# Kernel tuning notes

Measured on AMD Instinct MI355X. Metric: run time of the kernel, lower is better.

Reference implementation:

```python
import jax, jax.numpy as jnp
import numpy as np

N = 300000
MAX_TORSION = 7
MAX_RIGID = 8
MAX_SS = 3
MAX_ATOM = 24
NRES = 22
EPS = 1e-6


def v_norm_safe(v):
    # normalize last dim with epsilon clamp (torch v_norm_safe analogue)
    return v / jnp.clip(jnp.linalg.norm(v, axis=-1, keepdims=True), EPS)


def combine_operations(X, Y):
    # X, Y: [..., 4, 3] rigid ops (3x3 rotation rows + 1 translation row)
    rot = X[..., :3, :] @ Y[..., :3, :]
    t = jnp.einsum('...ij,...j->...i', X[..., :3, :], Y[..., 3, :]) + X[..., 3, :]
    return jnp.concatenate([rot, t[..., None, :]], axis=-2)


def setup_inputs() -> dict:
    key = jax.random.key(0)
    ks = jax.random.split(key, 9)
    return {
        'output_0': jax.random.normal(ks[0], (N, 2 * MAX_TORSION + MAX_SS, 1), jnp.float32),
        'output_1': jax.random.normal(ks[1], (N, 3, 3), jnp.float32),
        'pos': jax.random.normal(ks[2], (N, 3), jnp.float32),
        'ss': jax.random.randint(ks[3], (N,), 0, MAX_SS),
        'residue_type': jax.random.randint(ks[4], (N,), 0, NRES),
        'rigid_transforms': jax.random.normal(ks[5], (MAX_SS, NRES, MAX_RIGID, 4, 3), jnp.float32),
        'rigid_groups': jax.random.normal(ks[6], (MAX_SS, NRES, MAX_ATOM, 3), jnp.float32),
        'transforms_dep': jax.random.randint(ks[7], (NRES, MAX_RIGID), 0, MAX_RIGID),
        'rigids_dep': jax.random.randint(ks[8], (NRES, MAX_ATOM), 0, MAX_RIGID),
    }


def reference(output_0, output_1, pos, ss, residue_type,
              rigid_transforms, rigid_groups, transforms_dep, rigids_dep):
    # ---- StructureModule.output_to_opr_6D ----
    bb0 = output_1[:, :2]                                   # [N,2,3]
    e0 = v_norm_safe(bb0[:, 0])
    v1 = bb0[:, 1]
    u1 = v1 - e0 * jnp.sum(e0 * v1, axis=-1, keepdims=True)
    e1 = v_norm_safe(u1)
    e2 = jnp.cross(e0, e1)
    rot = jnp.stack([e0, e1, e2], axis=1).swapaxes(-1, -2)  # [N,3,3]
    t = 0.1 * output_1[:, 2][:, None, :]                    # [N,1,3]
    bb = jnp.concatenate([rot, t], axis=1)                  # [N,4,3]
    sc = v_norm_safe(output_0[:, :2 * MAX_TORSION].reshape(-1, MAX_TORSION, 2))

    # ---- build_structure ----
    transforms = rigid_transforms[ss, residue_type]         # [N,8,4,3]
    rigids = rigid_groups[ss, residue_type]                 # [N,24,3]
    tdep = transforms_dep[residue_type]                     # [N,8]
    rdep = rigids_dep[residue_type]                         # [N,24]

    n = output_0.shape[0]
    c, s = sc[..., 0], sc[..., 1]                           # [N,7]
    zr = jnp.zeros_like(c)
    on = jnp.ones_like(c)
    tor_rot = jnp.stack([
        jnp.stack([on, zr, zr], axis=-1),
        jnp.stack([zr, c, -s], axis=-1),
        jnp.stack([zr, s, c], axis=-1),
    ], axis=-2)                                             # [N,7,3,3]
    tor = jnp.concatenate(
        [tor_rot, jnp.zeros((n, MAX_TORSION, 1, 3), output_0.dtype)], axis=2)
    opr0 = jnp.concatenate([bb[:, :3], (bb[:, 3] + pos)[:, None]], axis=1)  # [N,4,3]
    opr = jnp.concatenate([opr0[:, None], tor], axis=1)     # [N,8,4,3]

    opr = combine_operations(transforms, opr)
    for i_tor in range(1, MAX_RIGID):                       # fixed 7-step dependency chain
        prev = jnp.take_along_axis(opr, tdep[:, i_tor][:, None, None, None], axis=1)[:, 0]
        opr = opr.at[:, i_tor].set(combine_operations(prev, opr[:, i_tor]))

    opr_g = jnp.take_along_axis(opr, rdep[:, :, None, None], axis=1)  # [N,24,4,3]
    R = jnp.einsum('naij,naj->nai', opr_g[:, :, :3], rigids) + opr_g[:, :, 3]
    return (R, opr[:, 0])
```

## Files before the change

### kernel.cpp

```cpp
#include <hip/hip_runtime.h>
#include <math.h>

#define NRES 22

__device__ __forceinline__ void sel8(const float (&fr)[8][12], int d, float (&P)[12]) {
    const bool b0 = (d & 1) != 0;
    const bool b1 = (d & 2) != 0;
    const bool b2 = (d & 4) != 0;
#pragma unroll
    for (int k = 0; k < 12; ++k) {
        float a01 = b0 ? fr[1][k] : fr[0][k];
        float a23 = b0 ? fr[3][k] : fr[2][k];
        float a45 = b0 ? fr[5][k] : fr[4][k];
        float a67 = b0 ? fr[7][k] : fr[6][k];
        float b03 = b1 ? a23 : a01;
        float b47 = b1 ? a67 : a45;
        P[k] = b2 ? b47 : b03;
    }
}

__device__ __forceinline__ void apply_point(const float (&F)[12], float x, float y, float z,
                                            float &px, float &py, float &pz) {
    px = fmaf(F[0], x, fmaf(F[1], y, fmaf(F[2], z, F[9])));
    py = fmaf(F[3], x, fmaf(F[4], y, fmaf(F[5], z, F[10])));
    pz = fmaf(F[6], x, fmaf(F[7], y, fmaf(F[8], z, F[11])));
}

extern "C" __global__ __launch_bounds__(256)
void model_kernel(const float* __restrict__ o0,
                  const float* __restrict__ o1,
                  const float* __restrict__ pos,
                  const int*   __restrict__ ssArr,
                  const int*   __restrict__ rtArr,
                  const float* __restrict__ rigT,
                  const float* __restrict__ rigG,
                  const int*   __restrict__ tdepArr,
                  const int*   __restrict__ rdepArr,
                  float* __restrict__ outR,
                  float* __restrict__ outF,
                  int N)
{
    const int res = blockIdx.x * 256 + threadIdx.x;
    if (res >= N) return;

    const int s  = ssArr[res];
    const int rt = rtArr[res];

    float c[7], sn[7];
    const float* o0p = o0 + (size_t)res * 17;
#pragma unroll
    for (int t = 0; t < 7; ++t) {
        float cr = o0p[2 * t], sr = o0p[2 * t + 1];
        float n2 = cr * cr + sr * sr;
        float inv = rsqrtf(fmaxf(n2, 1e-12f));
        c[t]  = cr * inv;
        sn[t] = sr * inv;
    }

    const float* o1p = o1 + (size_t)res * 9;
    float r0x = o1p[0], r0y = o1p[1], r0z = o1p[2];
    float v1x = o1p[3], v1y = o1p[4], v1z = o1p[5];
    float t2x = o1p[6], t2y = o1p[7], t2z = o1p[8];
    float inv0 = rsqrtf(fmaxf(r0x * r0x + r0y * r0y + r0z * r0z, 1e-12f));
    float e0x = r0x * inv0, e0y = r0y * inv0, e0z = r0z * inv0;
    float d01 = e0x * v1x + e0y * v1y + e0z * v1z;
    float u1x = v1x - e0x * d01, u1y = v1y - e0y * d01, u1z = v1z - e0z * d01;
    float inv1 = rsqrtf(fmaxf(u1x * u1x + u1y * u1y + u1z * u1z, 1e-12f));
    float e1x = u1x * inv1, e1y = u1y * inv1, e1z = u1z * inv1;
    float e2x = e0y * e1z - e0z * e1y;
    float e2y = e0z * e1x - e0x * e1z;
    float e2z = e0x * e1y - e0y * e1x;
    const float* pp = pos + (size_t)res * 3;
    float btx = 0.1f * t2x + pp[0];
    float bty = 0.1f * t2y + pp[1];
    float btz = 0.1f * t2z + pp[2];

    const int sr22 = s * NRES + rt;
    const float4* T4 = (const float4*)rigT + (size_t)sr22 * 24;

    float fr[8][12];

    {
        float4 q0 = T4[0], q1 = T4[1], q2 = T4[2];
        float T0[12] = {q0.x, q0.y, q0.z, q0.w, q1.x, q1.y, q1.z, q1.w,
                        q2.x, q2.y, q2.z, q2.w};
#pragma unroll
        for (int i = 0; i < 3; ++i) {
            float a = T0[i * 3 + 0], b = T0[i * 3 + 1], d = T0[i * 3 + 2];
            fr[0][i * 3 + 0] = a * e0x + b * e0y + d * e0z;
            fr[0][i * 3 + 1] = a * e1x + b * e1y + d * e1z;
            fr[0][i * 3 + 2] = a * e2x + b * e2y + d * e2z;
            fr[0][9 + i]     = a * btx + b * bty + d * btz + T0[9 + i];
        }
    }

#pragma unroll
    for (int f = 1; f < 8; ++f) {
        float4 q0 = T4[f * 3 + 0], q1 = T4[f * 3 + 1], q2 = T4[f * 3 + 2];
        float Tf[12] = {q0.x, q0.y, q0.z, q0.w, q1.x, q1.y, q1.z, q1.w,
                        q2.x, q2.y, q2.z, q2.w};
        float cc = c[f - 1], ssn = sn[f - 1];
#pragma unroll
        for (int i = 0; i < 3; ++i) {
            fr[f][i * 3 + 0] = Tf[i * 3 + 0];
            fr[f][i * 3 + 1] = Tf[i * 3 + 1] * cc + Tf[i * 3 + 2] * ssn;
            fr[f][i * 3 + 2] = Tf[i * 3 + 2] * cc - Tf[i * 3 + 1] * ssn;
            fr[f][9 + i]     = Tf[9 + i];
        }
    }

    int tdv[8];
    {
        const int4* tdq = (const int4*)(tdepArr + rt * 8);
        int4 a = tdq[0], b = tdq[1];
        tdv[0] = a.x; tdv[1] = a.y; tdv[2] = a.z; tdv[3] = a.w;
        tdv[4] = b.x; tdv[5] = b.y; tdv[6] = b.z; tdv[7] = b.w;
    }
#pragma unroll
    for (int i = 1; i < 8; ++i) {
        float P[12];
        sel8(fr, tdv[i] & 7, P);
        float Y[12];
#pragma unroll
        for (int k = 0; k < 12; ++k) Y[k] = fr[i][k];
#pragma unroll
        for (int r = 0; r < 3; ++r) {
            float a = P[r * 3 + 0], b = P[r * 3 + 1], d = P[r * 3 + 2];
#pragma unroll
            for (int j = 0; j < 3; ++j)
                fr[i][r * 3 + j] = a * Y[j] + b * Y[3 + j] + d * Y[6 + j];
            fr[i][9 + r] = a * Y[9] + b * Y[10] + d * Y[11] + P[9 + r];
        }
    }

    const float4* G4  = (const float4*)rigG + (size_t)sr22 * 18;
    const int4*   RD4 = (const int4*)(rdepArr + rt * 24);
    float4* OR4 = (float4*)(outR + (size_t)res * 72);
#pragma unroll
    for (int ck = 0; ck < 6; ++ck) {
        int4 rd = RD4[ck];
        float4 g0 = G4[ck * 3 + 0], g1 = G4[ck * 3 + 1], g2 = G4[ck * 3 + 2];
        float P[12];
        float p0x, p0y, p0z, p1x, p1y, p1z, p2x, p2y, p2z, p3x, p3y, p3z;
        sel8(fr, rd.x & 7, P); apply_point(P, g0.x, g0.y, g0.z, p0x, p0y, p0z);
        sel8(fr, rd.y & 7, P); apply_point(P, g0.w, g1.x, g1.y, p1x, p1y, p1z);
        sel8(fr, rd.z & 7, P); apply_point(P, g1.z, g1.w, g2.x, p2x, p2y, p2z);
        sel8(fr, rd.w & 7, P); apply_point(P, g2.y, g2.z, g2.w, p3x, p3y, p3z);
        OR4[ck * 3 + 0] = make_float4(p0x, p0y, p0z, p1x);
        OR4[ck * 3 + 1] = make_float4(p1y, p1z, p2x, p2y);
        OR4[ck * 3 + 2] = make_float4(p2z, p3x, p3y, p3z);
    }

    float4* OF4 = (float4*)(outF + (size_t)res * 12);
    OF4[0] = make_float4(fr[0][0], fr[0][1], fr[0][2], fr[0][3]);
    OF4[1] = make_float4(fr[0][4], fr[0][5], fr[0][6], fr[0][7]);
    OF4[2] = make_float4(fr[0][8], fr[0][9], fr[0][10], fr[0][11]);
}

extern "C" void kernel_launch(void* const* d_in, const int* in_sizes, int n_in,
                              void* d_out, int out_size, void* d_ws, size_t ws_size,
                              hipStream_t stream) {
    const float* o0   = (const float*)d_in[0];
    const float* o1   = (const float*)d_in[1];
    const float* pos  = (const float*)d_in[2];
    const int*   ssA  = (const int*)d_in[3];
    const int*   rtA  = (const int*)d_in[4];
    const float* rigT = (const float*)d_in[5];
    const float* rigG = (const float*)d_in[6];
    const int*   tdep = (const int*)d_in[7];
    const int*   rdep = (const int*)d_in[8];

    const int N = in_sizes[3];
    float* outR = (float*)d_out;
    float* outF = (float*)d_out + (size_t)N * 72;

    const int block = 256;
    const int grid  = (N + block - 1) / block;
    model_kernel<<<grid, block, 0, stream>>>(o0, o1, pos, ssA, rtA, rigT, rigG,
                                             tdep, rdep, outR, outF, N);
}
```

Measured before the change: 187.0 us.

## Stage lookup tables and per-wave I/O through LDS with persistent grid

Copies the rigid transform, rigid group and dependency tables into padded shared memory once per block, and runs a persistent grid-stride loop capped at 512 blocks. Each wave stages its residues' input rows into LDS with coalesced float4 loads, and transposes its output rows through LDS so global stores are coalesced instead of strided per thread. This targets uncoalesced per-thread global access, at the cost of about 80KB of LDS per block, extra LDS traffic and reduced occupancy.

```diff
diff --git a/kernel.cpp b/kernel.cpp
--- a/kernel.cpp
+++ b/kernel.cpp
@@ -2,6 +2,14 @@
 #include <math.h>
 
 #define NRES 22
+
+#define ST_F    0
+#define SG_F    6600
+#define STD_I   11616
+#define SRD_I   11814
+#define TBL_F   12364
+#define CHUNK_F 1856
+#define SMEM_BYTES ((TBL_F + 4 * CHUNK_F) * 4)
 
 __device__ __forceinline__ void sel8(const float (&fr)[8][12], int d, float (&P)[12]) {
     const bool b0 = (d & 1) != 0;
@@ -26,7 +34,20 @@
     pz = fmaf(F[6], x, fmaf(F[7], y, fmaf(F[8], z, F[11])));
 }
 
-extern "C" __global__ __launch_bounds__(256)
+__device__ __forceinline__ void wave_stage(const float* __restrict__ src, float* dst,
+                                           int nF, int lane) {
+    const int n4 = nF >> 2;
+    const float4* s4 = (const float4*)src;
+    float4* d4 = (float4*)dst;
+    for (int i = lane; i < n4; i += 64) d4[i] = s4[i];
+    const int rem = nF & 3;
+    if (lane < rem) {
+        const int b = n4 << 2;
+        dst[b + lane] = src[b + lane];
+    }
+}
+
+extern "C" __global__ __launch_bounds__(256, 2)
 void model_kernel(const float* __restrict__ o0,
                   const float* __restrict__ o1,
                   const float* __restrict__ pos,
@@ -40,121 +61,188 @@
                   float* __restrict__ outF,
                   int N)
 {
-    const int res = blockIdx.x * 256 + threadIdx.x;
-    if (res >= N) return;
-
-    const int s  = ssArr[res];
-    const int rt = rtArr[res];
-
-    float c[7], sn[7];
-    const float* o0p = o0 + (size_t)res * 17;
-#pragma unroll
-    for (int t = 0; t < 7; ++t) {
-        float cr = o0p[2 * t], sr = o0p[2 * t + 1];
-        float n2 = cr * cr + sr * sr;
-        float inv = rsqrtf(fmaxf(n2, 1e-12f));
-        c[t]  = cr * inv;
-        sn[t] = sr * inv;
-    }
-
-    const float* o1p = o1 + (size_t)res * 9;
-    float r0x = o1p[0], r0y = o1p[1], r0z = o1p[2];
-    float v1x = o1p[3], v1y = o1p[4], v1z = o1p[5];
-    float t2x = o1p[6], t2y = o1p[7], t2z = o1p[8];
-    float inv0 = rsqrtf(fmaxf(r0x * r0x + r0y * r0y + r0z * r0z, 1e-12f));
-    float e0x = r0x * inv0, e0y = r0y * inv0, e0z = r0z * inv0;
-    float d01 = e0x * v1x + e0y * v1y + e0z * v1z;
-    float u1x = v1x - e0x * d01, u1y = v1y - e0y * d01, u1z = v1z - e0z * d01;
-    float inv1 = rsqrtf(fmaxf(u1x * u1x + u1y * u1y + u1z * u1z, 1e-12f));
-    float e1x = u1x * inv1, e1y = u1y * inv1, e1z = u1z * inv1;
-    float e2x = e0y * e1z - e0z * e1y;
-    float e2y = e0z * e1x - e0x * e1z;
-    float e2z = e0x * e1y - e0y * e1x;
-    const float* pp = pos + (size_t)res * 3;
-    float btx = 0.1f * t2x + pp[0];
-    float bty = 0.1f * t2y + pp[1];
-    float btz = 0.1f * t2z + pp[2];
-
-    const int sr22 = s * NRES + rt;
-    const float4* T4 = (const float4*)rigT + (size_t)sr22 * 24;
-
-    float fr[8][12];
+    extern __shared__ __align__(16) float smem[];
+    int* smemI = (int*)smem;
+    const int tid  = threadIdx.x;
+    const int lane = tid & 63;
+    const int wave = tid >> 6;
 
     {
-        float4 q0 = T4[0], q1 = T4[1], q2 = T4[2];
-        float T0[12] = {q0.x, q0.y, q0.z, q0.w, q1.x, q1.y, q1.z, q1.w,
-                        q2.x, q2.y, q2.z, q2.w};
-#pragma unroll
-        for (int i = 0; i < 3; ++i) {
-            float a = T0[i * 3 + 0], b = T0[i * 3 + 1], d = T0[i * 3 + 2];
-            fr[0][i * 3 + 0] = a * e0x + b * e0y + d * e0z;
-            fr[0][i * 3 + 1] = a * e1x + b * e1y + d * e1z;
-            fr[0][i * 3 + 2] = a * e2x + b * e2y + d * e2z;
-            fr[0][9 + i]     = a * btx + b * bty + d * btz + T0[9 + i];
-        }
-    }
-
-#pragma unroll
-    for (int f = 1; f < 8; ++f) {
-        float4 q0 = T4[f * 3 + 0], q1 = T4[f * 3 + 1], q2 = T4[f * 3 + 2];
-        float Tf[12] = {q0.x, q0.y, q0.z, q0.w, q1.x, q1.y, q1.z, q1.w,
-                        q2.x, q2.y, q2.z, q2.w};
-        float cc = c[f - 1], ssn = sn[f - 1];
-#pragma unroll
-        for (int i = 0; i < 3; ++i) {
-            fr[f][i * 3 + 0] = Tf[i * 3 + 0];
-            fr[f][i * 3 + 1] = Tf[i * 3 + 1] * cc + Tf[i * 3 + 2] * ssn;
-            fr[f][i * 3 + 2] = Tf[i * 3 + 2] * cc - Tf[i * 3 + 1] * ssn;
-            fr[f][9 + i]     = Tf[9 + i];
-        }
-    }
-
-    int tdv[8];
+        const float4* s4 = (const float4*)rigT;
+        for (int t = tid; t < 1584; t += 256) {
+            float4 v = s4[t];
+            int rec = t / 24;
+            int k   = (t - rec * 24) << 2;
+            *(float4*)(smem + ST_F + rec * 100 + k) = v;
+        }
+    }
     {
-        const int4* tdq = (const int4*)(tdepArr + rt * 8);
-        int4 a = tdq[0], b = tdq[1];
-        tdv[0] = a.x; tdv[1] = a.y; tdv[2] = a.z; tdv[3] = a.w;
-        tdv[4] = b.x; tdv[5] = b.y; tdv[6] = b.z; tdv[7] = b.w;
-    }
-#pragma unroll
-    for (int i = 1; i < 8; ++i) {
-        float P[12];
-        sel8(fr, tdv[i] & 7, P);
-        float Y[12];
-#pragma unroll
-        for (int k = 0; k < 12; ++k) Y[k] = fr[i][k];
-#pragma unroll
-        for (int r = 0; r < 3; ++r) {
-            float a = P[r * 3 + 0], b = P[r * 3 + 1], d = P[r * 3 + 2];
-#pragma unroll
-            for (int j = 0; j < 3; ++j)
-                fr[i][r * 3 + j] = a * Y[j] + b * Y[3 + j] + d * Y[6 + j];
-            fr[i][9 + r] = a * Y[9] + b * Y[10] + d * Y[11] + P[9 + r];
-        }
-    }
-
-    const float4* G4  = (const float4*)rigG + (size_t)sr22 * 18;
-    const int4*   RD4 = (const int4*)(rdepArr + rt * 24);
-    float4* OR4 = (float4*)(outR + (size_t)res * 72);
-#pragma unroll
-    for (int ck = 0; ck < 6; ++ck) {
-        int4 rd = RD4[ck];
-        float4 g0 = G4[ck * 3 + 0], g1 = G4[ck * 3 + 1], g2 = G4[ck * 3 + 2];
-        float P[12];
-        float p0x, p0y, p0z, p1x, p1y, p1z, p2x, p2y, p2z, p3x, p3y, p3z;
-        sel8(fr, rd.x & 7, P); apply_point(P, g0.x, g0.y, g0.z, p0x, p0y, p0z);
-        sel8(fr, rd.y & 7, P); apply_point(P, g0.w, g1.x, g1.y, p1x, p1y, p1z);
-        sel8(fr, rd.z & 7, P); apply_point(P, g1.z, g1.w, g2.x, p2x, p2y, p2z);
-        sel8(fr, rd.w & 7, P); apply_point(P, g2.y, g2.z, g2.w, p3x, p3y, p3z);
-        OR4[ck * 3 + 0] = make_float4(p0x, p0y, p0z, p1x);
-        OR4[ck * 3 + 1] = make_float4(p1y, p1z, p2x, p2y);
-        OR4[ck * 3 + 2] = make_float4(p2z, p3x, p3y, p3z);
-    }
-
-    float4* OF4 = (float4*)(outF + (size_t)res * 12);
-    OF4[0] = make_float4(fr[0][0], fr[0][1], fr[0][2], fr[0][3]);
-    OF4[1] = make_float4(fr[0][4], fr[0][5], fr[0][6], fr[0][7]);
-    OF4[2] = make_float4(fr[0][8], fr[0][9], fr[0][10], fr[0][11]);
+        const float4* s4 = (const float4*)rigG;
+        for (int t = tid; t < 1188; t += 256) {
+            float4 v = s4[t];
+            int rec = t / 18;
+            int k   = (t - rec * 18) << 2;
+            *(float4*)(smem + SG_F + rec * 76 + k) = v;
+        }
+    }
+    for (int t = tid; t < 176; t += 256)
+        smemI[STD_I + (t >> 3) * 9 + (t & 7)] = tdepArr[t];
+    for (int t = tid; t < 528; t += 256) {
+        int r = t / 24;
+        smemI[SRD_I + r * 25 + (t - r * 24)] = rdepArr[t];
+    }
+    __syncthreads();
+
+    float* chunk = smem + TBL_F + wave * CHUNK_F;
+    const int gstride = (int)gridDim.x * 256;
+
+    for (int base = (int)blockIdx.x * 256; base < N; base += gstride) {
+        const int wres0 = base + wave * 64;
+        const int cnt   = min(64, N - wres0);
+
+        asm volatile("s_waitcnt lgkmcnt(0)" ::: "memory");
+
+        if (cnt > 0) {
+            wave_stage(o0  + (size_t)wres0 * 17, chunk,        cnt * 17, lane);
+            wave_stage(o1  + (size_t)wres0 * 9,  chunk + 1088, cnt * 9,  lane);
+            wave_stage(pos + (size_t)wres0 * 3,  chunk + 1664, cnt * 3,  lane);
+        }
+        asm volatile("s_waitcnt lgkmcnt(0)" ::: "memory");
+
+        const int  res   = wres0 + lane;
+        const bool alive = (lane < cnt);
+
+        float  fr[8][12];
+        float4 out4[18];
+
+        if (alive) {
+            const int s    = ssArr[res];
+            const int rt   = rtArr[res];
+            const int sr22 = s * NRES + rt;
+
+            const float* myo0 = chunk + lane * 17;
+            float c[7], sn[7];
+#pragma unroll
+            for (int t = 0; t < 7; ++t) {
+                float cr = myo0[2 * t], sr = myo0[2 * t + 1];
+                float inv = rsqrtf(fmaxf(cr * cr + sr * sr, 1e-12f));
+                c[t]  = cr * inv;
+                sn[t] = sr * inv;
+            }
+
+            const float* myo1 = chunk + 1088 + lane * 9;
+            float r0x = myo1[0], r0y = myo1[1], r0z = myo1[2];
+            float v1x = myo1[3], v1y = myo1[4], v1z = myo1[5];
+            float t2x = myo1[6], t2y = myo1[7], t2z = myo1[8];
+            float inv0 = rsqrtf(fmaxf(r0x * r0x + r0y * r0y + r0z * r0z, 1e-12f));
+            float e0x = r0x * inv0, e0y = r0y * inv0, e0z = r0z * inv0;
+            float d01 = e0x * v1x + e0y * v1y + e0z * v1z;
+            float u1x = v1x - e0x * d01, u1y = v1y - e0y * d01, u1z = v1z - e0z * d01;
+            float inv1 = rsqrtf(fmaxf(u1x * u1x + u1y * u1y + u1z * u1z, 1e-12f));
+            float e1x = u1x * inv1, e1y = u1y * inv1, e1z = u1z * inv1;
+            float e2x = e0y * e1z - e0z * e1y;
+            float e2y = e0z * e1x - e0x * e1z;
+            float e2z = e0x * e1y - e0y * e1x;
+            const float* myp = chunk + 1664 + lane * 3;
+            float btx = 0.1f * t2x + myp[0];
+            float bty = 0.1f * t2y + myp[1];
+            float btz = 0.1f * t2z + myp[2];
+
+            const float4* T4 = (const float4*)smem + sr22 * 25;
+
+            {
+                float4 q0 = T4[0], q1 = T4[1], q2 = T4[2];
+                float T0[12] = {q0.x, q0.y, q0.z, q0.w, q1.x, q1.y, q1.z, q1.w,
+                                q2.x, q2.y, q2.z, q2.w};
+#pragma unroll
+                for (int i = 0; i < 3; ++i) {
+                    float a = T0[i * 3 + 0], b = T0[i * 3 + 1], d = T0[i * 3 + 2];
+                    fr[0][i * 3 + 0] = a * e0x + b * e0y + d * e0z;
+                    fr[0][i * 3 + 1] = a * e1x + b * e1y + d * e1z;
+                    fr[0][i * 3 + 2] = a * e2x + b * e2y + d * e2z;
+                    fr[0][9 + i]     = a * btx + b * bty + d * btz + T0[9 + i];
+                }
+            }
+
+#pragma unroll
+            for (int f = 1; f < 8; ++f) {
+                float4 q0 = T4[f * 3 + 0], q1 = T4[f * 3 + 1], q2 = T4[f * 3 + 2];
+                float Tf[12] = {q0.x, q0.y, q0.z, q0.w, q1.x, q1.y, q1.z, q1.w,
+                                q2.x, q2.y, q2.z, q2.w};
+                float cc = c[f - 1], ssn = sn[f - 1];
+#pragma unroll
+                for (int i = 0; i < 3; ++i) {
+                    fr[f][i * 3 + 0] = Tf[i * 3 + 0];
+                    fr[f][i * 3 + 1] = Tf[i * 3 + 1] * cc + Tf[i * 3 + 2] * ssn;
+                    fr[f][i * 3 + 2] = Tf[i * 3 + 2] * cc - Tf[i * 3 + 1] * ssn;
+                    fr[f][9 + i]     = Tf[9 + i];
+                }
+            }
+
+            const int* tdp = smemI + STD_I + rt * 9;
+#pragma unroll
+            for (int i = 1; i < 8; ++i) {
+                float P[12];
+                sel8(fr, tdp[i] & 7, P);
+                float Y[12];
+#pragma unroll
+                for (int k = 0; k < 12; ++k) Y[k] = fr[i][k];
+#pragma unroll
+                for (int r = 0; r < 3; ++r) {
+                    float a = P[r * 3 + 0], b = P[r * 3 + 1], d = P[r * 3 + 2];
+#pragma unroll
+                    for (int j = 0; j < 3; ++j)
+                        fr[i][r * 3 + j] = a * Y[j] + b * Y[3 + j] + d * Y[6 + j];
+                    fr[i][9 + r] = a * Y[9] + b * Y[10] + d * Y[11] + P[9 + r];
+                }
+            }
+
+            float4* OF4 = (float4*)outF + (size_t)res * 3;
+            OF4[0] = make_float4(fr[0][0], fr[0][1], fr[0][2], fr[0][3]);
+            OF4[1] = make_float4(fr[0][4], fr[0][5], fr[0][6], fr[0][7]);
+            OF4[2] = make_float4(fr[0][8], fr[0][9], fr[0][10], fr[0][11]);
+
+            const float4* G4  = (const float4*)smem + 1650 + sr22 * 19;
+            const int*    rdp = smemI + SRD_I + rt * 25;
+#pragma unroll
+            for (int ck = 0; ck < 6; ++ck) {
+                int d0 = rdp[ck * 4 + 0] & 7, d1 = rdp[ck * 4 + 1] & 7;
+                int d2 = rdp[ck * 4 + 2] & 7, d3 = rdp[ck * 4 + 3] & 7;
+                float4 g0 = G4[ck * 3 + 0], g1 = G4[ck * 3 + 1], g2 = G4[ck * 3 + 2];
+                float P[12];
+                float p0x, p0y, p0z, p1x, p1y, p1z, p2x, p2y, p2z, p3x, p3y, p3z;
+                sel8(fr, d0, P); apply_point(P, g0.x, g0.y, g0.z, p0x, p0y, p0z);
+                sel8(fr, d1, P); apply_point(P, g0.w, g1.x, g1.y, p1x, p1y, p1z);
+                sel8(fr, d2, P); apply_point(P, g1.z, g1.w, g2.x, p2x, p2y, p2z);
+                sel8(fr, d3, P); apply_point(P, g2.y, g2.z, g2.w, p3x, p3y, p3z);
+                out4[ck * 3 + 0] = make_float4(p0x, p0y, p0z, p1x);
+                out4[ck * 3 + 1] = make_float4(p1y, p1z, p2x, p2y);
+                out4[ck * 3 + 2] = make_float4(p2z, p3x, p3y, p3z);
+            }
+        }
+
+#pragma unroll 1
+        for (int r = 0; r < 4; ++r) {
+            const int rb = wres0 + r * 16;
+            const int vr = min(16, N - rb);
+            if (vr > 0) {
+                asm volatile("s_waitcnt lgkmcnt(0)" ::: "memory");
+                if ((lane >> 4) == r && (lane & 15) < vr) {
+                    float4* slotp = (float4*)(chunk + (lane & 15) * 76);
+#pragma unroll
+                    for (int j = 0; j < 18; ++j) slotp[j] = out4[j];
+                }
+                asm volatile("s_waitcnt lgkmcnt(0)" ::: "memory");
+                const float4* c4  = (const float4*)chunk;
+                float4*       dst = (float4*)outR + (size_t)rb * 18;
+                const int     n4r = vr * 18;
+                for (int i = lane; i < n4r; i += 64) {
+                    int slot = i / 18;
+                    dst[i] = c4[slot * 19 + (i - slot * 18)];
+                }
+            }
+        }
+    }
 }
 
 extern "C" void kernel_launch(void* const* d_in, const int* in_sizes, int n_in,
@@ -174,8 +262,15 @@
     float* outR = (float*)d_out;
     float* outF = (float*)d_out + (size_t)N * 72;
 
-    const int block = 256;
-    const int grid  = (N + block - 1) / block;
-    model_kernel<<<grid, block, 0, stream>>>(o0, o1, pos, ssA, rtA, rigT, rigG,
-                                             tdep, rdep, outR, outF, N);
-}
+    static bool attr_set = false;
+    if (!attr_set) {
+        hipFuncSetAttribute((const void*)model_kernel,
+                            hipFuncAttributeMaxDynamicSharedMemorySize, SMEM_BYTES);
+        attr_set = true;
+    }
+
+    int grid = (N + 255) / 256;
+    if (grid > 512) grid = 512;
+    model_kernel<<<grid, 256, SMEM_BYTES, stream>>>(o0, o1, pos, ssA, rtA, rigT, rigG,
+                                                    tdep, rdep, outR, outF, N);
+}
```

Measured after the change: 182.7 us. -2.3%, faster.
